# Performance work log

Hardware: AMD Instinct MI355X
Metric: run time of the kernel (lower is better)

Reference implementation:

```python
import jax, jax.numpy as jnp
import numpy as np

NUM_ADC_P = 8           # num_of_adc_p
L_TILDE = 64            # num_samples_L_tilde
DENSE_L = 1024          # params.dense_sampling_L
GAUSS_STD = 10.0        # params.gaussian_sampling_std


def setup_inputs() -> dict:
    key = jax.random.key(0)
    kx, = jax.random.split(key, 1)
    B = 16384
    x = jax.random.normal(kx, (B, NUM_ADC_P * DENSE_L), dtype=jnp.float32)
    # learned sample positions, init = linspace(0, L, L_tilde+2)[1:-1]
    start = np.linspace(0.0, DENSE_L, L_TILDE + 2, dtype=np.float64)[1:-1]
    weight = jnp.asarray(start, dtype=jnp.float32)
    return {"x": x, "weight": weight}


def reference(x, weight):
    B = x.shape[0]
    dt = x.dtype
    t = jnp.arange(1, DENSE_L + 1, dtype=dt)                      # [L]
    # Gaussian weighting matrix shared across all ADC channels: [L, L_tilde]
    W = jnp.exp(-((t[:, None] - weight[None, :].astype(dt)) ** 2) / (GAUSS_STD ** 2))
    xb = x.reshape(B, NUM_ADC_P, DENSE_L)                         # [B, P, L]
    out = jnp.einsum('bpl,lk->bpk', xb, W)                        # [B, P, L_tilde]
    return out.reshape(B, NUM_ADC_P * L_TILDE)
```

## Files before the change

### kernel.cpp

```cpp
#include <hip/hip_runtime.h>
#include <hip/hip_bf16.h>

#define NUM_ADC_P 8
#define DENSE_L   1024
#define L_TILDE   64

typedef __attribute__((ext_vector_type(8))) short  short8;
typedef __attribute__((ext_vector_type(4))) float  float4v;


__global__ void build_w(const float* __restrict__ weight,
                        __hip_bfloat16* __restrict__ wt) {
    const int n = blockIdx.x;
    const float wn = weight[n];
    for (int k = threadIdx.x; k < DENSE_L; k += blockDim.x) {
        const float t = (float)(k + 1);
        const float d = t - wn;
        wt[n * DENSE_L + k] = __float2bfloat16(expf(-d * d * 0.01f));
    }
}

__device__ __forceinline__ short8 cvt8(float4v a, float4v b) {
    union { short8 s; __hip_bfloat162 h[4]; } u;
    u.h[0] = __float22bfloat162_rn(make_float2(a[0], a[1]));
    u.h[1] = __float22bfloat162_rn(make_float2(a[2], a[3]));
    u.h[2] = __float22bfloat162_rn(make_float2(b[0], b[1]));
    u.h[3] = __float22bfloat162_rn(make_float2(b[2], b[3]));
    return u.s;
}

__device__ __forceinline__ float4v ldnt(const float* p) {
    return __builtin_nontemporal_load((const float4v*)p);
}

__global__ __launch_bounds__(256, 4)
void sampling_gemm(const float* __restrict__ x,
                   const __hip_bfloat16* __restrict__ wt,
                   float* __restrict__ out) {
    const int lane = threadIdx.x & 63;
    const int wave = threadIdx.x >> 6;
    const int r    = lane & 15;
    const int q    = lane >> 4;

    const long m0 = (long)blockIdx.x * 128 + (long)wave * 32;

    const float* a0 = x + (m0 + r) * DENSE_L + q * 8;
    const float* a1 = a0 + 16 * DENSE_L;
    const short* w0 = (const short*)wt + r * DENSE_L + q * 8;

    float4v acc[2][4];
    #pragma unroll
    for (int i = 0; i < 2; ++i)
        #pragma unroll
        for (int j = 0; j < 4; ++j)
            acc[i][j] = (float4v){0.f, 0.f, 0.f, 0.f};

    float4v c0a = ldnt(a0), c0b = ldnt(a0 + 4);
    float4v c1a = ldnt(a1), c1b = ldnt(a1 + 4);

    for (int kk = 0; kk < 32; ++kk) {
        const short* wk = w0 + kk * 32;
        const short8 b0 = *(const short8*)(wk);
        const short8 b1 = *(const short8*)(wk + 16 * DENSE_L);
        const short8 b2 = *(const short8*)(wk + 32 * DENSE_L);
        const short8 b3 = *(const short8*)(wk + 48 * DENSE_L);

        const int kn = (kk + 1) & 31;
        const float4v n0a = ldnt(a0 + kn * 32);
        const float4v n0b = ldnt(a0 + kn * 32 + 4);
        const float4v n1a = ldnt(a1 + kn * 32);
        const float4v n1b = ldnt(a1 + kn * 32 + 4);

        const short8 af0 = cvt8(c0a, c0b);
        const short8 af1 = cvt8(c1a, c1b);

        acc[0][0] = __builtin_amdgcn_mfma_f32_16x16x32_bf16(af0, b0, acc[0][0], 0, 0, 0);
        acc[1][0] = __builtin_amdgcn_mfma_f32_16x16x32_bf16(af1, b0, acc[1][0], 0, 0, 0);
        acc[0][1] = __builtin_amdgcn_mfma_f32_16x16x32_bf16(af0, b1, acc[0][1], 0, 0, 0);
        acc[1][1] = __builtin_amdgcn_mfma_f32_16x16x32_bf16(af1, b1, acc[1][1], 0, 0, 0);
        acc[0][2] = __builtin_amdgcn_mfma_f32_16x16x32_bf16(af0, b2, acc[0][2], 0, 0, 0);
        acc[1][2] = __builtin_amdgcn_mfma_f32_16x16x32_bf16(af1, b2, acc[1][2], 0, 0, 0);
        acc[0][3] = __builtin_amdgcn_mfma_f32_16x16x32_bf16(af0, b3, acc[0][3], 0, 0, 0);
        acc[1][3] = __builtin_amdgcn_mfma_f32_16x16x32_bf16(af1, b3, acc[1][3], 0, 0, 0);

        c0a = n0a; c0b = n0b; c1a = n1a; c1b = n1b;
    }

    #pragma unroll
    for (int ms = 0; ms < 2; ++ms) {
        #pragma unroll
        for (int ns = 0; ns < 4; ++ns) {
            #pragma unroll
            for (int rr = 0; rr < 4; ++rr) {
                __builtin_nontemporal_store(
                    acc[ms][ns][rr],
                    out + (m0 + ms * 16 + q * 4 + rr) * L_TILDE + ns * 16 + r);
            }
        }
    }
}

extern "C" void kernel_launch(void* const* d_in, const int* in_sizes, int n_in,
                              void* d_out, int out_size, void* d_ws, size_t ws_size,
                              hipStream_t stream) {
    const float* x      = (const float*)d_in[0];
    const float* weight = (const float*)d_in[1];
    float* out          = (float*)d_out;
    __hip_bfloat16* wt  = (__hip_bfloat16*)d_ws;

    const int M = in_sizes[0] / DENSE_L;
    const int grid = M / 128;

    build_w<<<64, 256, 0, stream>>>(weight, wt);
    sampling_gemm<<<grid, 256, 0, stream>>>(x, wt, out);
}
```

Measured before the change: 719.3 us.

## Stage x tiles through LDS with async global_load_lds double buffering

Replaces per-lane register prefetch of x with direct global-to-LDS loads into a double-buffered 64x128 tile, so the next K chunk is fetched while the current one feeds MFMA. The block tile drops from 128 to 64 rows, each wave covering 16 rows, and B fragments for four K substeps are loaded at once. The goal is better overlap and coalescing of the HBM stream in this memory-bound GEMM. In exchange it uses 64KB of LDS per block, lowers occupancy, adds a block barrier per step, and halves per-wave reuse of W fragments.

```diff
diff --git a/kernel.cpp b/kernel.cpp
--- a/kernel.cpp
+++ b/kernel.cpp
@@ -4,6 +4,10 @@
 #define NUM_ADC_P 8
 #define DENSE_L   1024
 #define L_TILDE   64
+
+#define M_TILE    64
+#define K_STEP    128
+#define N_STEPS   (DENSE_L / K_STEP)
 
 typedef __attribute__((ext_vector_type(8))) short  short8;
 typedef __attribute__((ext_vector_type(4))) float  float4v;
@@ -29,73 +33,85 @@
     return u.s;
 }
 
-__device__ __forceinline__ float4v ldnt(const float* p) {
-    return __builtin_nontemporal_load((const float4v*)p);
+__device__ __forceinline__ void gload_lds16(const float* src, float* lds_dst) {
+    __builtin_amdgcn_global_load_lds(
+        (const __attribute__((address_space(1))) unsigned int*)src,
+        (__attribute__((address_space(3))) unsigned int*)lds_dst,
+        16, 0, 0);
 }
 
-__global__ __launch_bounds__(256, 4)
+__global__ __launch_bounds__(256, 2)
 void sampling_gemm(const float* __restrict__ x,
                    const __hip_bfloat16* __restrict__ wt,
                    float* __restrict__ out) {
+    __shared__ float A_lds[2][M_TILE * K_STEP];
+
     const int lane = threadIdx.x & 63;
-    const int wave = threadIdx.x >> 6;
+    const int w    = threadIdx.x >> 6;
     const int r    = lane & 15;
     const int q    = lane >> 4;
+    const int half = lane >> 5;
+    const int lc   = lane & 31;
 
-    const long m0 = (long)blockIdx.x * 128 + (long)wave * 32;
+    const long m0 = (long)blockIdx.x * M_TILE;
+    const long mw = m0 + (long)w * 16;
 
-    const float* a0 = x + (m0 + r) * DENSE_L + q * 8;
-    const float* a1 = a0 + 16 * DENSE_L;
     const short* w0 = (const short*)wt + r * DENSE_L + q * 8;
 
-    float4v acc[2][4];
+    float4v acc[4];
     #pragma unroll
-    for (int i = 0; i < 2; ++i)
+    for (int n = 0; n < 4; ++n) acc[n] = (float4v){0.f, 0.f, 0.f, 0.f};
+
+    auto stage = [&](int step, int buf) {
         #pragma unroll
-        for (int j = 0; j < 4; ++j)
-            acc[i][j] = (float4v){0.f, 0.f, 0.f, 0.f};
+        for (int i = 0; i < 8; ++i) {
+            const long row = mw + i * 2 + half;
+            const float* src = x + row * DENSE_L + step * K_STEP + lc * 4;
+            float* dst = &A_lds[buf][(w * 16 + i * 2) * K_STEP];
+            gload_lds16(src, dst);
+        }
+    };
 
-    float4v c0a = ldnt(a0), c0b = ldnt(a0 + 4);
-    float4v c1a = ldnt(a1), c1b = ldnt(a1 + 4);
+    stage(0, 0);
+    __syncthreads();
 
-    for (int kk = 0; kk < 32; ++kk) {
-        const short* wk = w0 + kk * 32;
-        const short8 b0 = *(const short8*)(wk);
-        const short8 b1 = *(const short8*)(wk + 16 * DENSE_L);
-        const short8 b2 = *(const short8*)(wk + 32 * DENSE_L);
-        const short8 b3 = *(const short8*)(wk + 48 * DENSE_L);
+    int cur = 0;
+    for (int step = 0; step < N_STEPS; ++step) {
+        short8 bfr[4][4];
+        #pragma unroll
+        for (int s = 0; s < 4; ++s) {
+            const short* wk = w0 + (step * 4 + s) * 32;
+            #pragma unroll
+            for (int n = 0; n < 4; ++n)
+                bfr[s][n] = *(const short8*)(wk + n * 16 * DENSE_L);
+        }
 
-        const int kn = (kk + 1) & 31;
-        const float4v n0a = ldnt(a0 + kn * 32);
-        const float4v n0b = ldnt(a0 + kn * 32 + 4);
-        const float4v n1a = ldnt(a1 + kn * 32);
-        const float4v n1b = ldnt(a1 + kn * 32 + 4);
+        if (step < N_STEPS - 1)
+            stage(step + 1, cur ^ 1);
 
-        const short8 af0 = cvt8(c0a, c0b);
-        const short8 af1 = cvt8(c1a, c1b);
+        #pragma unroll
+        for (int s = 0; s < 4; ++s) {
+            const float* ap = &A_lds[cur][(w * 16 + r) * K_STEP + s * 32 + q * 8];
+            const float4v alo = *(const float4v*)ap;
+            const float4v ahi = *(const float4v*)(ap + 4);
+            const short8 af = cvt8(alo, ahi);
+            acc[0] = __builtin_amdgcn_mfma_f32_16x16x32_bf16(af, bfr[s][0], acc[0], 0, 0, 0);
+            acc[1] = __builtin_amdgcn_mfma_f32_16x16x32_bf16(af, bfr[s][1], acc[1], 0, 0, 0);
+            acc[2] = __builtin_amdgcn_mfma_f32_16x16x32_bf16(af, bfr[s][2], acc[2], 0, 0, 0);
+            acc[3] = __builtin_amdgcn_mfma_f32_16x16x32_bf16(af, bfr[s][3], acc[3], 0, 0, 0);
+        }
 
-        acc[0][0] = __builtin_amdgcn_mfma_f32_16x16x32_bf16(af0, b0, acc[0][0], 0, 0, 0);
-        acc[1][0] = __builtin_amdgcn_mfma_f32_16x16x32_bf16(af1, b0, acc[1][0], 0, 0, 0);
-        acc[0][1] = __builtin_amdgcn_mfma_f32_16x16x32_bf16(af0, b1, acc[0][1], 0, 0, 0);
-        acc[1][1] = __builtin_amdgcn_mfma_f32_16x16x32_bf16(af1, b1, acc[1][1], 0, 0, 0);
-        acc[0][2] = __builtin_amdgcn_mfma_f32_16x16x32_bf16(af0, b2, acc[0][2], 0, 0, 0);
-        acc[1][2] = __builtin_amdgcn_mfma_f32_16x16x32_bf16(af1, b2, acc[1][2], 0, 0, 0);
-        acc[0][3] = __builtin_amdgcn_mfma_f32_16x16x32_bf16(af0, b3, acc[0][3], 0, 0, 0);
-        acc[1][3] = __builtin_amdgcn_mfma_f32_16x16x32_bf16(af1, b3, acc[1][3], 0, 0, 0);
-
-        c0a = n0a; c0b = n0b; c1a = n1a; c1b = n1b;
+        __syncthreads();
+        cur ^= 1;
     }
 
     #pragma unroll
-    for (int ms = 0; ms < 2; ++ms) {
+    for (int ns = 0; ns < 4; ++ns) {
         #pragma unroll
-        for (int ns = 0; ns < 4; ++ns) {
-            #pragma unroll
-            for (int rr = 0; rr < 4; ++rr) {
-                __builtin_nontemporal_store(
-                    acc[ms][ns][rr],
-                    out + (m0 + ms * 16 + q * 4 + rr) * L_TILDE + ns * 16 + r);
-            }
+        for (int rr = 0; rr < 4; ++rr) {
+            __builtin_nontemporal_store(
+                acc[ns][rr],
+                out + (mw + q * 4 + rr) * L_TILDE + ns * 16 + r);
         }
     }
 }
@@ -109,7 +125,7 @@
     __hip_bfloat16* wt  = (__hip_bfloat16*)d_ws;
 
     const int M = in_sizes[0] / DENSE_L;
-    const int grid = M / 128;
+    const int grid = M / M_TILE;
 
     build_w<<<64, 256, 0, stream>>>(weight, wt);
     sampling_gemm<<<grid, 256, 0, stream>>>(x, wt, out);
```

After: 724.3 us. About the same (+0.7%).

## Fuse Gaussian weight build into GEMM via swizzled LDS and larger blocks

Applied to the files above, without the earlier changes.

Drops the separate build_w kernel. Each 1024-thread block now computes the full bf16 Gaussian weight matrix into 128KB of XOR-swizzled shared memory, and the MFMA loop reads B fragments from LDS instead of global memory. The main loop is also unrolled to prefetch two K-steps of x ahead, and each block now handles 512 rows. The aim is to remove strided global loads of the weight matrix and one kernel launch. The cost is redundant exp work in every block, one block per CU because of the LDS footprint, and register pressure from the aggressive launch bounds.

```diff
diff --git a/kernel.cpp b/kernel.cpp
--- a/kernel.cpp
+++ b/kernel.cpp
@@ -5,20 +5,12 @@
 #define DENSE_L   1024
 #define L_TILDE   64
 
+#define M_PER_BLOCK 512
+#define THREADS     1024
+
 typedef __attribute__((ext_vector_type(8))) short  short8;
 typedef __attribute__((ext_vector_type(4))) float  float4v;
 
-
-__global__ void build_w(const float* __restrict__ weight,
-                        __hip_bfloat16* __restrict__ wt) {
-    const int n = blockIdx.x;
-    const float wn = weight[n];
-    for (int k = threadIdx.x; k < DENSE_L; k += blockDim.x) {
-        const float t = (float)(k + 1);
-        const float d = t - wn;
-        wt[n * DENSE_L + k] = __float2bfloat16(expf(-d * d * 0.01f));
-    }
-}
 
 __device__ __forceinline__ short8 cvt8(float4v a, float4v b) {
     union { short8 s; __hip_bfloat162 h[4]; } u;
@@ -33,20 +25,42 @@
     return __builtin_nontemporal_load((const float4v*)p);
 }
 
-__global__ __launch_bounds__(256, 4)
+__global__ __launch_bounds__(THREADS, 4)
 void sampling_gemm(const float* __restrict__ x,
-                   const __hip_bfloat16* __restrict__ wt,
+                   const float* __restrict__ weight,
                    float* __restrict__ out) {
-    const int lane = threadIdx.x & 63;
-    const int wave = threadIdx.x >> 6;
+    __shared__ short Wt[64 * DENSE_L];
+    char* wtb = (char*)Wt;
+
+    const int tid = threadIdx.x;
+
+    {
+        const int n  = tid >> 4;
+        const int k0 = (tid & 15) * 64;
+        const float wn = weight[n];
+        const int xr = (n & 7) << 4;
+        #pragma unroll 8
+        for (int j = 0; j < 64; ++j) {
+            const int k = k0 + j;
+            const float d = (float)(k + 1) - wn;
+            const int byte = (n * 2048 + k * 2) ^ xr;
+            *(__hip_bfloat16*)(wtb + byte) = __float2bfloat16(expf(-d * d * 0.01f));
+        }
+    }
+    __syncthreads();
+
+    const int lane = tid & 63;
+    const int wave = tid >> 6;
     const int r    = lane & 15;
     const int q    = lane >> 4;
 
-    const long m0 = (long)blockIdx.x * 128 + (long)wave * 32;
+    const long m0 = (long)blockIdx.x * M_PER_BLOCK + (long)wave * 32;
 
     const float* a0 = x + (m0 + r) * DENSE_L + q * 8;
     const float* a1 = a0 + 16 * DENSE_L;
-    const short* w0 = (const short*)wt + r * DENSE_L + q * 8;
+
+    const int xmask = (r & 7) << 4;
+    const int bbase = r * 2048 + q * 16;
 
     float4v acc[2][4];
     #pragma unroll
@@ -55,35 +69,60 @@
         for (int j = 0; j < 4; ++j)
             acc[i][j] = (float4v){0.f, 0.f, 0.f, 0.f};
 
-    float4v c0a = ldnt(a0), c0b = ldnt(a0 + 4);
-    float4v c1a = ldnt(a1), c1b = ldnt(a1 + 4);
+    float4v e0a = ldnt(a0),      e0b = ldnt(a0 + 4);
+    float4v e1a = ldnt(a1),      e1b = ldnt(a1 + 4);
+    float4v o0a = ldnt(a0 + 32), o0b = ldnt(a0 + 36);
+    float4v o1a = ldnt(a1 + 32), o1b = ldnt(a1 + 36);
 
-    for (int kk = 0; kk < 32; ++kk) {
-        const short* wk = w0 + kk * 32;
-        const short8 b0 = *(const short8*)(wk);
-        const short8 b1 = *(const short8*)(wk + 16 * DENSE_L);
-        const short8 b2 = *(const short8*)(wk + 32 * DENSE_L);
-        const short8 b3 = *(const short8*)(wk + 48 * DENSE_L);
-
-        const int kn = (kk + 1) & 31;
-        const float4v n0a = ldnt(a0 + kn * 32);
-        const float4v n0b = ldnt(a0 + kn * 32 + 4);
-        const float4v n1a = ldnt(a1 + kn * 32);
-        const float4v n1b = ldnt(a1 + kn * 32 + 4);
-
-        const short8 af0 = cvt8(c0a, c0b);
-        const short8 af1 = cvt8(c1a, c1b);
-
-        acc[0][0] = __builtin_amdgcn_mfma_f32_16x16x32_bf16(af0, b0, acc[0][0], 0, 0, 0);
-        acc[1][0] = __builtin_amdgcn_mfma_f32_16x16x32_bf16(af1, b0, acc[1][0], 0, 0, 0);
-        acc[0][1] = __builtin_amdgcn_mfma_f32_16x16x32_bf16(af0, b1, acc[0][1], 0, 0, 0);
-        acc[1][1] = __builtin_amdgcn_mfma_f32_16x16x32_bf16(af1, b1, acc[1][1], 0, 0, 0);
-        acc[0][2] = __builtin_amdgcn_mfma_f32_16x16x32_bf16(af0, b2, acc[0][2], 0, 0, 0);
-        acc[1][2] = __builtin_amdgcn_mfma_f32_16x16x32_bf16(af1, b2, acc[1][2], 0, 0, 0);
-        acc[0][3] = __builtin_amdgcn_mfma_f32_16x16x32_bf16(af0, b3, acc[0][3], 0, 0, 0);
-        acc[1][3] = __builtin_amdgcn_mfma_f32_16x16x32_bf16(af1, b3, acc[1][3], 0, 0, 0);
-
-        c0a = n0a; c0b = n0b; c1a = n1a; c1b = n1b;
+    for (int t = 0; t < 30; t += 2) {
+        {
+            const short8 af0 = cvt8(e0a, e0b);
+            const short8 af1 = cvt8(e1a, e1b);
+            e0a = ldnt(a0 + (t + 2) * 32); e0b = ldnt(a0 + (t + 2) * 32 + 4);
+            e1a = ldnt(a1 + (t + 2) * 32); e1b = ldnt(a1 + (t + 2) * 32 + 4);
+            #pragma unroll
+            for (int ns = 0; ns < 4; ++ns) {
+                const short8 bf = *(const short8*)(
+                    wtb + ((bbase + ns * 32768 + t * 64) ^ xmask));
+                acc[0][ns] = __builtin_amdgcn_mfma_f32_16x16x32_bf16(af0, bf, acc[0][ns], 0, 0, 0);
+                acc[1][ns] = __builtin_amdgcn_mfma_f32_16x16x32_bf16(af1, bf, acc[1][ns], 0, 0, 0);
+            }
+        }
+        {
+            const short8 af0 = cvt8(o0a, o0b);
+            const short8 af1 = cvt8(o1a, o1b);
+            o0a = ldnt(a0 + (t + 3) * 32); o0b = ldnt(a0 + (t + 3) * 32 + 4);
+            o1a = ldnt(a1 + (t + 3) * 32); o1b = ldnt(a1 + (t + 3) * 32 + 4);
+            #pragma unroll
+            for (int ns = 0; ns < 4; ++ns) {
+                const short8 bf = *(const short8*)(
+                    wtb + ((bbase + ns * 32768 + (t + 1) * 64) ^ xmask));
+                acc[0][ns] = __builtin_amdgcn_mfma_f32_16x16x32_bf16(af0, bf, acc[0][ns], 0, 0, 0);
+                acc[1][ns] = __builtin_amdgcn_mfma_f32_16x16x32_bf16(af1, bf, acc[1][ns], 0, 0, 0);
+            }
+        }
+    }
+    {
+        const short8 af0 = cvt8(e0a, e0b);
+        const short8 af1 = cvt8(e1a, e1b);
+        #pragma unroll
+        for (int ns = 0; ns < 4; ++ns) {
+            const short8 bf = *(const short8*)(
+                wtb + ((bbase + ns * 32768 + 30 * 64) ^ xmask));
+            acc[0][ns] = __builtin_amdgcn_mfma_f32_16x16x32_bf16(af0, bf, acc[0][ns], 0, 0, 0);
+            acc[1][ns] = __builtin_amdgcn_mfma_f32_16x16x32_bf16(af1, bf, acc[1][ns], 0, 0, 0);
+        }
+    }
+    {
+        const short8 af0 = cvt8(o0a, o0b);
+        const short8 af1 = cvt8(o1a, o1b);
+        #pragma unroll
+        for (int ns = 0; ns < 4; ++ns) {
+            const short8 bf = *(const short8*)(
+                wtb + ((bbase + ns * 32768 + 31 * 64) ^ xmask));
+            acc[0][ns] = __builtin_amdgcn_mfma_f32_16x16x32_bf16(af0, bf, acc[0][ns], 0, 0, 0);
+            acc[1][ns] = __builtin_amdgcn_mfma_f32_16x16x32_bf16(af1, bf, acc[1][ns], 0, 0, 0);
+        }
     }
 
     #pragma unroll
@@ -106,11 +145,10 @@
     const float* x      = (const float*)d_in[0];
     const float* weight = (const float*)d_in[1];
     float* out          = (float*)d_out;
-    __hip_bfloat16* wt  = (__hip_bfloat16*)d_ws;
+    (void)d_ws; (void)ws_size;
 
     const int M = in_sizes[0] / DENSE_L;
-    const int grid = M / 128;
+    const int grid = M / M_PER_BLOCK;
 
-    build_w<<<64, 256, 0, stream>>>(weight, wt);
-    sampling_gemm<<<grid, 256, 0, stream>>>(x, wt, out);
+    sampling_gemm<<<grid, THREADS, 0, stream>>>(x, weight, out);
 }
```

Result: faster. 703.2 us (-2.2%).
